# Kernel optimization log

Measured on AMD Instinct MI355X. Metric: run time of the kernel, lower is better.

The kernel has to match this reference:

```python
import jax, jax.numpy as jnp
import numpy as np

B, S, D_IN, D_OUT, N_HEAD = 4, 2048, 1024, 1024, 16
D_HEAD = D_OUT // N_HEAD


def setup_inputs() -> dict:
    key = jax.random.key(0)
    k_x, k_wq, k_wo, k_bo = jax.random.split(key, 4)
    x = jax.random.normal(k_x, (B, S, D_IN), dtype=jnp.float32)
    # nn.Linear(d_in, d_out) weight is [d_out, d_in]; we store transposed [d_in, d_out]
    W_Q = jax.random.normal(k_wq, (D_IN, D_OUT), dtype=jnp.float32) * (D_IN ** -0.5)
    W_out = jax.random.normal(k_wo, (D_OUT, D_OUT), dtype=jnp.float32) * (D_OUT ** -0.5)
    b_out = jax.random.normal(k_bo, (D_OUT,), dtype=jnp.float32) * 0.01
    return {"x": x, "W_Q": W_Q, "W_out": W_out, "b_out": b_out}


def reference(x, W_Q, W_out, b_out):
    b, n_tok, _ = x.shape
    # Faithful to source: Q, K, V all use W_Q (source bug preserved)
    qkv = jnp.einsum('btd,de->bte', x, W_Q)  # [b, s, d_out]
    q = qkv.reshape(b, n_tok, N_HEAD, D_HEAD).transpose(0, 2, 1, 3)  # [b,h,s,dh]
    k = q
    v = q
    scores = jnp.einsum('bhqd,bhkd->bhqk', q, k)  # [b,h,s,s]
    causal = jnp.triu(jnp.ones((n_tok, n_tok), dtype=bool), k=1)
    scores = jnp.where(causal, -jnp.inf, scores)
    # source divides by sqrt(d_head) after masking; -inf / c == -inf so same result
    attn = jax.nn.softmax(scores / jnp.sqrt(jnp.float32(D_HEAD)), axis=-1)
    ctx = jnp.einsum('bhqk,bhkd->bhqd', attn, v)  # [b,h,s,dh]
    ctx = ctx.transpose(0, 2, 1, 3).reshape(b, n_tok, D_OUT)
    return jnp.einsum('btd,de->bte', ctx, W_out) + b_out
```

## Files before the change

kernel.cpp:

```cpp
#include <hip/hip_runtime.h>
#include <hip/hip_bf16.h>
#include <math.h>

#define B_ 4
#define S_ 2048
#define NH_ 16
#define DH_ 64
#define DM_ 1024

typedef __attribute__((ext_vector_type(4))) float f32x4;
typedef __attribute__((ext_vector_type(8))) short s16x8;
typedef __attribute__((ext_vector_type(4))) short s16x4;
typedef __attribute__((ext_vector_type(2))) unsigned u32x2;

extern "C" __device__ float __ocml_native_exp2_f32(float);
static __device__ __forceinline__ float nexp2(float x) {
  return __ocml_native_exp2_f32(x);
}

static __device__ __forceinline__ short f2bf(float f) {
  union { float f; unsigned u; } c; c.f = f;
  unsigned r = c.u + 0x7fffu + ((c.u >> 16) & 1u);
  return (short)(r >> 16);
}

static __device__ __forceinline__ unsigned pkbf(float a, float b) {
  union { __hip_bfloat162 h; unsigned u; } cv;
  cv.h = __float22bfloat162_rn(make_float2(a, b));
  return cv.u;
}

static __device__ __forceinline__ unsigned pkbf_fast(float a, float b) {
  unsigned r;
  asm("v_cvt_pk_bf16_f32 %0, %1, %2" : "=v"(r) : "v"(a), "v"(b));
  return r;
}

static __device__ __forceinline__ s16x4 mk4(unsigned lo, unsigned hi) {
  union { unsigned u[2]; s16x4 v; } x; x.u[0] = lo; x.u[1] = hi; return x.v;
}

#if __has_builtin(__builtin_amdgcn_mfma_f32_16x16x16bf16_1k)
#define HAVE16 1
static __device__ __forceinline__ f32x4 pv_mfma(s16x4 a, s16x4 b, f32x4 c) {
  return __builtin_amdgcn_mfma_f32_16x16x16bf16_1k(a, b, c, 0, 0, 0);
}
#else
#define HAVE16 0
static __device__ __forceinline__ f32x4 pv_mfma(s16x4 a, s16x4 b, f32x4 c) {
  asm volatile("v_mfma_f32_16x16x16_bf16 %0, %1, %2, %0" : "+v"(c) : "v"(a), "v"(b));
  return c;
}
#endif

static __device__ __forceinline__ void gload16(const void* g, void* l) {
  __builtin_amdgcn_global_load_lds(
      (const __attribute__((address_space(1))) void*)g,
      (__attribute__((address_space(3))) void*)l, 16, 0, 0);
}

__global__ void cvt_kernel(const float* __restrict__ in, short* __restrict__ out) {
  int i = (blockIdx.x * 256 + threadIdx.x) * 8;
  f32x4 a = *(const f32x4*)(in + i);
  f32x4 b = *(const f32x4*)(in + i + 4);
  s16x8 o;
  o[0] = f2bf(a[0]); o[1] = f2bf(a[1]); o[2] = f2bf(a[2]); o[3] = f2bf(a[3]);
  o[4] = f2bf(b[0]); o[5] = f2bf(b[1]); o[6] = f2bf(b[2]); o[7] = f2bf(b[3]);
  *(s16x8*)(out + i) = o;
}

__global__ void tcvt_kernel(const float* __restrict__ W, short* __restrict__ WT) {
  __shared__ float t[32][33];
  int tx = threadIdx.x & 31, ty = threadIdx.x >> 5;
  int bn = blockIdx.x * 32, bk = blockIdx.y * 32;
#pragma unroll
  for (int r = 0; r < 32; r += 8)
    t[ty + r][tx] = W[(size_t)(bk + ty + r) * DM_ + bn + tx];
  __syncthreads();
#pragma unroll
  for (int r = 0; r < 32; r += 8)
    WT[(size_t)(bn + ty + r) * DM_ + bk + tx] = f2bf(t[tx][ty + r]);
}

template <int EPI>
__global__ __launch_bounds__(256, 2) void gemm_kernel(
    const short* __restrict__ A, const short* __restrict__ BT,
    void* __restrict__ Cout, short* __restrict__ CoutT,
    const float* __restrict__ bias) {
  __shared__ short Al[128 * 64];
  __shared__ short Bl[128 * 64];
  const int tid = threadIdx.x;
  const int wid = tid >> 6, lane = tid & 63;
  const int l15 = lane & 15, l4 = lane >> 4;
  const int bm = blockIdx.y * 128, bn = blockIdx.x * 128;
  const int wm = (wid >> 1) * 64, wn = (wid & 1) * 64;
  f32x4 acc[4][4] = {};

  for (int kt = 0; kt < DM_; kt += 64) {
    __syncthreads();
#pragma unroll
    for (int j = 0; j < 4; ++j) {
      int s = j * 256 + tid;
      int row = s >> 3;
      int sl = (s & 7) ^ (row & 7);
      gload16(A + (size_t)(bm + row) * DM_ + kt + sl * 8, &Al[j * 2048 + wid * 512]);
    }
#pragma unroll
    for (int j = 0; j < 4; ++j) {
      int s = j * 256 + tid;
      int row = s >> 3;
      int sl = (s & 7) ^ (row & 7);
      gload16(BT + (size_t)(bn + row) * DM_ + kt + sl * 8, &Bl[j * 2048 + wid * 512]);
    }
    __syncthreads();
#pragma unroll
    for (int kk = 0; kk < 2; ++kk) {
      s16x8 af[4], bfr[4];
#pragma unroll
      for (int mi = 0; mi < 4; ++mi) {
        int row = wm + mi * 16 + l15;
        int sl = (kk * 4 + l4) ^ (row & 7);
        af[mi] = *(const s16x8*)&Al[row * 64 + sl * 8];
      }
#pragma unroll
      for (int ni = 0; ni < 4; ++ni) {
        int row = wn + ni * 16 + l15;
        int sl = (kk * 4 + l4) ^ (row & 7);
        bfr[ni] = *(const s16x8*)&Bl[row * 64 + sl * 8];
      }
#pragma unroll
      for (int mi = 0; mi < 4; ++mi)
#pragma unroll
        for (int ni = 0; ni < 4; ++ni)
          acc[mi][ni] = __builtin_amdgcn_mfma_f32_16x16x32_bf16(af[mi], bfr[ni], acc[mi][ni], 0, 0, 0);
    }
  }

  if (EPI == 0) {
    const float sc = 0.42466089786f;
    short* Q = (short*)Cout;
#pragma unroll
    for (int mi = 0; mi < 4; ++mi)
#pragma unroll
      for (int ni = 0; ni < 4; ++ni) {
        int rr0 = bm + wm + mi * 16 + l4 * 4;
        int cc = bn + wn + ni * 16 + l15;
        int b = rr0 >> 11, s0 = rr0 & 2047, h = cc >> 6, d = cc & 63;
        int bh = b * NH_ + h;
        float v0 = acc[mi][ni][0] * sc, v1 = acc[mi][ni][1] * sc;
        float v2 = acc[mi][ni][2] * sc, v3 = acc[mi][ni][3] * sc;
        Q[(((size_t)bh * S_ + s0 + 0) << 6) + d] = f2bf(v0);
        Q[(((size_t)bh * S_ + s0 + 1) << 6) + d] = f2bf(v1);
        Q[(((size_t)bh * S_ + s0 + 2) << 6) + d] = f2bf(v2);
        Q[(((size_t)bh * S_ + s0 + 3) << 6) + d] = f2bf(v3);
        u32x2 pk;
        pk[0] = pkbf(v0, v1);
        pk[1] = pkbf(v2, v3);
        *(u32x2*)&CoutT[(((size_t)bh * DH_ + d) << 11) + s0] = pk;
      }
  } else {
    float* O = (float*)Cout;
#pragma unroll
    for (int mi = 0; mi < 4; ++mi)
#pragma unroll
      for (int ni = 0; ni < 4; ++ni)
#pragma unroll
        for (int r = 0; r < 4; ++r) {
          int rr = bm + wm + mi * 16 + l4 * 4 + r;
          int cc = bn + wn + ni * 16 + l15;
          O[(size_t)rr * DM_ + cc] = acc[mi][ni][r] + bias[cc];
        }
  }
}

__global__ __launch_bounds__(256, 4) void attn_kernel(
    const short* __restrict__ Qb, const short* __restrict__ QbT,
    short* __restrict__ Ctx) {
  __shared__ short Kl[2][64 * 64];
  __shared__ short Vt[2][64 * 64];
  const int tid = threadIdx.x;
  const int wid = tid >> 6, lane = tid & 63;
  const int l15 = lane & 15, l4 = lane >> 4;
  const int bid = blockIdx.x;
  const int bh = bid & 63;
  const int g = bid >> 6;
  const int qt = (int)((0x32104567ba98cdefULL >> (g * 4)) & 15);
  const short* Qh = Qb + (size_t)bh * S_ * DH_;
  const short* QTh = QbT + (size_t)bh * DH_ * S_;
  const int q0 = qt * 128 + wid * 32;

  s16x8 aq[2][2];
#pragma unroll
  for (int qi = 0; qi < 2; ++qi)
#pragma unroll
    for (int kk = 0; kk < 2; ++kk)
      aq[qi][kk] = *(const s16x8*)(Qh + (size_t)(q0 + qi * 16 + l15) * DH_ + kk * 32 + l4 * 8);

  f32x4 acc_o[4][2] = {};
  f32x4 lacc[2] = {};
  s16x4 ones;
  ones[0] = (short)0x3F80; ones[1] = (short)0x3F80;
  ones[2] = (short)0x3F80; ones[3] = (short)0x3F80;

  const int e7 = l15 & 7;
  const int ka0 = l15 * 64 + ((l4) ^ e7) * 8;
  const int ka1 = l15 * 64 + ((4 + l4) ^ e7) * 8;
  int vtoff[4];
#pragma unroll
  for (int ki = 0; ki < 4; ++ki)
    vtoff[ki] = l15 * 64 + (((ki * 2 + (l4 >> 1)) ^ e7) << 3) + (l4 & 1) * 4;

  const int c0 = wid * 64 + lane, c1 = c0 + 256;
  const int r0 = c0 >> 3, s0 = (c0 & 7) ^ (r0 & 7);
  const int r1 = c1 >> 3, s1 = (c1 & 7) ^ (r1 & 7);
  const short* pK0 = Qh + r0 * 64 + s0 * 8;
  const short* pK1 = Qh + r1 * 64 + s1 * 8;
  const short* pV0 = QTh + (size_t)r0 * S_ + s0 * 8;
  const short* pV1 = QTh + (size_t)r1 * S_ + s1 * 8;

  auto stage = [&](int buf) {
    gload16(pK0, &Kl[buf][wid * 512]);
    gload16(pK1, &Kl[buf][wid * 512 + 2048]);
    gload16(pV0, &Vt[buf][wid * 512]);
    gload16(pV1, &Vt[buf][wid * 512 + 2048]);
    pK0 += 4096; pK1 += 4096;
    pV0 += 64;   pV1 += 64;
  };

  stage(0);

  int cur = 0;
  const int nt = qt * 2 + 2;
  for (int t = 0; t < nt; ++t) {
    asm volatile("s_waitcnt vmcnt(0)" ::: "memory");
    __syncthreads();
    if (t + 1 < nt) stage(cur ^ 1);
    const int kv0 = t * 64;

    if (kv0 <= q0) {
      const short* kl = &Kl[cur][0];
      const short* vt = &Vt[cur][0];
      f32x4 sa[4][2] = {};
      __builtin_amdgcn_s_setprio(1);
#pragma unroll
      for (int kk = 0; kk < 2; ++kk) {
        const int kb = (kk == 0) ? ka0 : ka1;
        s16x8 ka[4];
#pragma unroll
        for (int ki = 0; ki < 4; ++ki)
          ka[ki] = *(const s16x8*)&kl[kb + ki * 1024];
#pragma unroll
        for (int ki = 0; ki < 4; ++ki)
#pragma unroll
          for (int qi = 0; qi < 2; ++qi)
            sa[ki][qi] = __builtin_amdgcn_mfma_f32_16x16x32_bf16(ka[ki], aq[qi][kk], sa[ki][qi], 0, 0, 0);
      }
      __builtin_amdgcn_s_setprio(0);
      if (kv0 + 63 > q0) {
#pragma unroll
        for (int ki = 0; ki < 4; ++ki)
#pragma unroll
          for (int qi = 0; qi < 2; ++qi)
#pragma unroll
            for (int r = 0; r < 4; ++r) {
              int kvg = kv0 + ki * 16 + l4 * 4 + r;
              int qg = q0 + qi * 16 + l15;
              if (kvg > qg) sa[ki][qi][r] = -INFINITY;
            }
      }
      unsigned pw[4][2][2];
#pragma unroll
      for (int ki = 0; ki < 4; ++ki)
#pragma unroll
        for (int qi = 0; qi < 2; ++qi) {
          float e0 = nexp2(sa[ki][qi][0]);
          float e1 = nexp2(sa[ki][qi][1]);
          float e2 = nexp2(sa[ki][qi][2]);
          float e3 = nexp2(sa[ki][qi][3]);
          pw[ki][qi][0] = pkbf_fast(e0, e1);
          pw[ki][qi][1] = pkbf_fast(e2, e3);
        }
      __builtin_amdgcn_s_setprio(1);
#pragma unroll
      for (int ki = 0; ki < 4; ++ki) {
        lacc[0] = pv_mfma(ones, mk4(pw[ki][0][0], pw[ki][0][1]), lacc[0]);
        lacc[1] = pv_mfma(ones, mk4(pw[ki][1][0], pw[ki][1][1]), lacc[1]);
      }
#pragma unroll
      for (int df = 0; df < 4; ++df) {
#pragma unroll
        for (int ki = 0; ki < 4; ++ki) {
          s16x4 av = *(const s16x4*)&vt[df * 1024 + vtoff[ki]];
          acc_o[df][0] = pv_mfma(av, mk4(pw[ki][0][0], pw[ki][0][1]), acc_o[df][0]);
          acc_o[df][1] = pv_mfma(av, mk4(pw[ki][1][0], pw[ki][1][1]), acc_o[df][1]);
        }
      }
      __builtin_amdgcn_s_setprio(0);
#if !HAVE16
      asm volatile("s_nop 7" :::);
      asm volatile("s_nop 7" :::);
#endif
    }
    cur ^= 1;
  }

  const int b = bh >> 4, h = bh & 15;
  const float ISQC = 2.35482208f;
  float inv[2] = {ISQC / lacc[0][0], ISQC / lacc[1][0]};
#pragma unroll
  for (int df = 0; df < 4; ++df)
#pragma unroll
    for (int qi = 0; qi < 2; ++qi) {
      int qg = q0 + qi * 16 + l15;
      int col = h * 64 + df * 16 + l4 * 4;
      u32x2 pk;
      pk[0] = pkbf_fast(acc_o[df][qi][0] * inv[qi], acc_o[df][qi][1] * inv[qi]);
      pk[1] = pkbf_fast(acc_o[df][qi][2] * inv[qi], acc_o[df][qi][3] * inv[qi]);
      *(u32x2*)&Ctx[(size_t)(b * S_ + qg) * DM_ + col] = pk;
    }
}

extern "C" void kernel_launch(void* const* d_in, const int* in_sizes, int n_in,
                              void* d_out, int out_size, void* d_ws, size_t ws_size,
                              hipStream_t stream) {
  const float* x  = (const float*)d_in[0];
  const float* Wq = (const float*)d_in[1];
  const float* Wo = (const float*)d_in[2];
  const float* bo = (const float*)d_in[3];
  float* out = (float*)d_out;
  char* ws = (char*)d_ws;

  short* xb  = (short*)(ws);
  short* WqT = (short*)(ws + 16777216);
  short* WoT = (short*)(ws + 18874368);
  short* Qb  = (short*)(ws + 20971520);
  short* QbT = (short*)(ws + 37748736);
  short* Ctx = xb;

  cvt_kernel<<<4096, 256, 0, stream>>>(x, xb);
  tcvt_kernel<<<dim3(32, 32), 256, 0, stream>>>(Wq, WqT);
  tcvt_kernel<<<dim3(32, 32), 256, 0, stream>>>(Wo, WoT);
  gemm_kernel<0><<<dim3(8, 64), 256, 0, stream>>>(xb, WqT, Qb, QbT, nullptr);
  attn_kernel<<<1024, 256, 0, stream>>>(Qb, QbT, Ctx);
  gemm_kernel<1><<<dim3(8, 64), 256, 0, stream>>>(Ctx, WoT, out, nullptr, bo);
}
```

Before: 122.2 us.

## Halve attention query tile to 64 rows and merge weight transpose launches

The attention kernel now gives each block 64 query rows (16 per wave) instead of 128 (32 per wave) and launches 2048 blocks, scheduled longest-first. This gives finer causal load balance and removes the per-wave skip branch. The cost is that each K/V tile loaded into LDS is reused by half as many queries, roughly doubling K/V traffic. The two weight transpose-convert launches are merged into one grid with a z dimension, and the Q epilogue reuses the packed hardware bf16 conversion instead of converting each value twice.

New measurement: 123.3 us. Within noise of the previous version (+0.9%).

```diff
diff --git a/kernel.cpp b/kernel.cpp
--- a/kernel.cpp
+++ b/kernel.cpp
@@ -22,12 +22,6 @@
   union { float f; unsigned u; } c; c.f = f;
   unsigned r = c.u + 0x7fffu + ((c.u >> 16) & 1u);
   return (short)(r >> 16);
-}
-
-static __device__ __forceinline__ unsigned pkbf(float a, float b) {
-  union { __hip_bfloat162 h; unsigned u; } cv;
-  cv.h = __float22bfloat162_rn(make_float2(a, b));
-  return cv.u;
 }
 
 static __device__ __forceinline__ unsigned pkbf_fast(float a, float b) {
@@ -69,8 +63,11 @@
   *(s16x8*)(out + i) = o;
 }
 
-__global__ void tcvt_kernel(const float* __restrict__ W, short* __restrict__ WT) {
+__global__ void tcvt_kernel(const float* __restrict__ W0, const float* __restrict__ W1,
+                            short* __restrict__ T0, short* __restrict__ T1) {
   __shared__ float t[32][33];
+  const float* W = blockIdx.z ? W1 : W0;
+  short* WT = blockIdx.z ? T1 : T0;
   int tx = threadIdx.x & 31, ty = threadIdx.x >> 5;
   int bn = blockIdx.x * 32, bk = blockIdx.y * 32;
 #pragma unroll
@@ -147,15 +144,13 @@
         int cc = bn + wn + ni * 16 + l15;
         int b = rr0 >> 11, s0 = rr0 & 2047, h = cc >> 6, d = cc & 63;
         int bh = b * NH_ + h;
-        float v0 = acc[mi][ni][0] * sc, v1 = acc[mi][ni][1] * sc;
-        float v2 = acc[mi][ni][2] * sc, v3 = acc[mi][ni][3] * sc;
-        Q[(((size_t)bh * S_ + s0 + 0) << 6) + d] = f2bf(v0);
-        Q[(((size_t)bh * S_ + s0 + 1) << 6) + d] = f2bf(v1);
-        Q[(((size_t)bh * S_ + s0 + 2) << 6) + d] = f2bf(v2);
-        Q[(((size_t)bh * S_ + s0 + 3) << 6) + d] = f2bf(v3);
         u32x2 pk;
-        pk[0] = pkbf(v0, v1);
-        pk[1] = pkbf(v2, v3);
+        pk[0] = pkbf_fast(acc[mi][ni][0] * sc, acc[mi][ni][1] * sc);
+        pk[1] = pkbf_fast(acc[mi][ni][2] * sc, acc[mi][ni][3] * sc);
+        Q[(((size_t)bh * S_ + s0 + 0) << 6) + d] = (short)(pk[0] & 0xffff);
+        Q[(((size_t)bh * S_ + s0 + 1) << 6) + d] = (short)(pk[0] >> 16);
+        Q[(((size_t)bh * S_ + s0 + 2) << 6) + d] = (short)(pk[1] & 0xffff);
+        Q[(((size_t)bh * S_ + s0 + 3) << 6) + d] = (short)(pk[1] >> 16);
         *(u32x2*)&CoutT[(((size_t)bh * DH_ + d) << 11) + s0] = pk;
       }
   } else {
@@ -183,21 +178,18 @@
   const int l15 = lane & 15, l4 = lane >> 4;
   const int bid = blockIdx.x;
   const int bh = bid & 63;
-  const int g = bid >> 6;
-  const int qt = (int)((0x32104567ba98cdefULL >> (g * 4)) & 15);
+  const int s = 31 - (bid >> 6);
   const short* Qh = Qb + (size_t)bh * S_ * DH_;
   const short* QTh = QbT + (size_t)bh * DH_ * S_;
-  const int q0 = qt * 128 + wid * 32;
-
-  s16x8 aq[2][2];
-#pragma unroll
-  for (int qi = 0; qi < 2; ++qi)
-#pragma unroll
-    for (int kk = 0; kk < 2; ++kk)
-      aq[qi][kk] = *(const s16x8*)(Qh + (size_t)(q0 + qi * 16 + l15) * DH_ + kk * 32 + l4 * 8);
-
-  f32x4 acc_o[4][2] = {};
-  f32x4 lacc[2] = {};
+  const int q0 = s * 64 + wid * 16;
+
+  s16x8 aq[2];
+#pragma unroll
+  for (int kk = 0; kk < 2; ++kk)
+    aq[kk] = *(const s16x8*)(Qh + (size_t)(q0 + l15) * DH_ + kk * 32 + l4 * 8);
+
+  f32x4 acc_o[4] = {};
+  f32x4 lacc = {};
   s16x4 ones;
   ones[0] = (short)0x3F80; ones[1] = (short)0x3F80;
   ones[2] = (short)0x3F80; ones[3] = (short)0x3F80;
@@ -230,94 +222,82 @@
   stage(0);
 
   int cur = 0;
-  const int nt = qt * 2 + 2;
+  const int nt = s + 1;
   for (int t = 0; t < nt; ++t) {
     asm volatile("s_waitcnt vmcnt(0)" ::: "memory");
     __syncthreads();
     if (t + 1 < nt) stage(cur ^ 1);
     const int kv0 = t * 64;
-
-    if (kv0 <= q0) {
-      const short* kl = &Kl[cur][0];
-      const short* vt = &Vt[cur][0];
-      f32x4 sa[4][2] = {};
-      __builtin_amdgcn_s_setprio(1);
-#pragma unroll
-      for (int kk = 0; kk < 2; ++kk) {
-        const int kb = (kk == 0) ? ka0 : ka1;
-        s16x8 ka[4];
-#pragma unroll
-        for (int ki = 0; ki < 4; ++ki)
-          ka[ki] = *(const s16x8*)&kl[kb + ki * 1024];
-#pragma unroll
-        for (int ki = 0; ki < 4; ++ki)
-#pragma unroll
-          for (int qi = 0; qi < 2; ++qi)
-            sa[ki][qi] = __builtin_amdgcn_mfma_f32_16x16x32_bf16(ka[ki], aq[qi][kk], sa[ki][qi], 0, 0, 0);
+    const short* kl = &Kl[cur][0];
+    const short* vt = &Vt[cur][0];
+
+    f32x4 sa[4] = {};
+    __builtin_amdgcn_s_setprio(1);
+#pragma unroll
+    for (int kk = 0; kk < 2; ++kk) {
+      const int kb = (kk == 0) ? ka0 : ka1;
+      s16x8 ka[4];
+#pragma unroll
+      for (int ki = 0; ki < 4; ++ki)
+        ka[ki] = *(const s16x8*)&kl[kb + ki * 1024];
+#pragma unroll
+      for (int ki = 0; ki < 4; ++ki)
+        sa[ki] = __builtin_amdgcn_mfma_f32_16x16x32_bf16(ka[ki], aq[kk], sa[ki], 0, 0, 0);
+    }
+    __builtin_amdgcn_s_setprio(0);
+
+    if (kv0 + 63 > q0) {
+      int qg = q0 + l15;
+#pragma unroll
+      for (int ki = 0; ki < 4; ++ki)
+#pragma unroll
+        for (int r = 0; r < 4; ++r)
+          if (kv0 + ki * 16 + l4 * 4 + r > qg) sa[ki][r] = -INFINITY;
+    }
+
+    unsigned pw[4][2];
+#pragma unroll
+    for (int ki = 0; ki < 4; ++ki) {
+      float e0 = nexp2(sa[ki][0]);
+      float e1 = nexp2(sa[ki][1]);
+      float e2 = nexp2(sa[ki][2]);
+      float e3 = nexp2(sa[ki][3]);
+      pw[ki][0] = pkbf_fast(e0, e1);
+      pw[ki][1] = pkbf_fast(e2, e3);
+    }
+
+    __builtin_amdgcn_s_setprio(1);
+#pragma unroll
+    for (int ki = 0; ki < 4; ++ki)
+      lacc = pv_mfma(ones, mk4(pw[ki][0], pw[ki][1]), lacc);
+#pragma unroll
+    for (int df = 0; df < 4; ++df) {
+#pragma unroll
+      for (int ki = 0; ki < 4; ++ki) {
+        s16x4 av = *(const s16x4*)&vt[df * 1024 + vtoff[ki]];
+        acc_o[df] = pv_mfma(av, mk4(pw[ki][0], pw[ki][1]), acc_o[df]);
       }
-      __builtin_amdgcn_s_setprio(0);
-      if (kv0 + 63 > q0) {
-#pragma unroll
-        for (int ki = 0; ki < 4; ++ki)
-#pragma unroll
-          for (int qi = 0; qi < 2; ++qi)
-#pragma unroll
-            for (int r = 0; r < 4; ++r) {
-              int kvg = kv0 + ki * 16 + l4 * 4 + r;
-              int qg = q0 + qi * 16 + l15;
-              if (kvg > qg) sa[ki][qi][r] = -INFINITY;
-            }
-      }
-      unsigned pw[4][2][2];
-#pragma unroll
-      for (int ki = 0; ki < 4; ++ki)
-#pragma unroll
-        for (int qi = 0; qi < 2; ++qi) {
-          float e0 = nexp2(sa[ki][qi][0]);
-          float e1 = nexp2(sa[ki][qi][1]);
-          float e2 = nexp2(sa[ki][qi][2]);
-          float e3 = nexp2(sa[ki][qi][3]);
-          pw[ki][qi][0] = pkbf_fast(e0, e1);
-          pw[ki][qi][1] = pkbf_fast(e2, e3);
-        }
-      __builtin_amdgcn_s_setprio(1);
-#pragma unroll
-      for (int ki = 0; ki < 4; ++ki) {
-        lacc[0] = pv_mfma(ones, mk4(pw[ki][0][0], pw[ki][0][1]), lacc[0]);
-        lacc[1] = pv_mfma(ones, mk4(pw[ki][1][0], pw[ki][1][1]), lacc[1]);
-      }
-#pragma unroll
-      for (int df = 0; df < 4; ++df) {
-#pragma unroll
-        for (int ki = 0; ki < 4; ++ki) {
-          s16x4 av = *(const s16x4*)&vt[df * 1024 + vtoff[ki]];
-          acc_o[df][0] = pv_mfma(av, mk4(pw[ki][0][0], pw[ki][0][1]), acc_o[df][0]);
-          acc_o[df][1] = pv_mfma(av, mk4(pw[ki][1][0], pw[ki][1][1]), acc_o[df][1]);
-        }
-      }
-      __builtin_amdgcn_s_setprio(0);
+    }
+    __builtin_amdgcn_s_setprio(0);
 #if !HAVE16
-      asm volatile("s_nop 7" :::);
-      asm volatile("s_nop 7" :::);
+    asm volatile("s_nop 7" :::);
+    asm volatile("s_nop 7" :::);
 #endif
-    }
     cur ^= 1;
   }
 
   const int b = bh >> 4, h = bh & 15;
   const float ISQC = 2.35482208f;
-  float inv[2] = {ISQC / lacc[0][0], ISQC / lacc[1][0]};
-#pragma unroll
-  for (int df = 0; df < 4; ++df)
-#pragma unroll
-    for (int qi = 0; qi < 2; ++qi) {
-      int qg = q0 + qi * 16 + l15;
-      int col = h * 64 + df * 16 + l4 * 4;
-      u32x2 pk;
-      pk[0] = pkbf_fast(acc_o[df][qi][0] * inv[qi], acc_o[df][qi][1] * inv[qi]);
-      pk[1] = pkbf_fast(acc_o[df][qi][2] * inv[qi], acc_o[df][qi][3] * inv[qi]);
-      *(u32x2*)&Ctx[(size_t)(b * S_ + qg) * DM_ + col] = pk;
-    }
+  float inv = ISQC / lacc[0];
+  int qg = q0 + l15;
+#pragma unroll
+  for (int df = 0; df < 4; ++df) {
+    int col = h * 64 + df * 16 + l4 * 4;
+    u32x2 pk;
+    pk[0] = pkbf_fast(acc_o[df][0] * inv, acc_o[df][1] * inv);
+    pk[1] = pkbf_fast(acc_o[df][2] * inv, acc_o[df][3] * inv);
+    *(u32x2*)&Ctx[(size_t)(b * S_ + qg) * DM_ + col] = pk;
+  }
 }
 
 extern "C" void kernel_launch(void* const* d_in, const int* in_sizes, int n_in,
@@ -338,9 +318,8 @@
   short* Ctx = xb;
 
   cvt_kernel<<<4096, 256, 0, stream>>>(x, xb);
-  tcvt_kernel<<<dim3(32, 32), 256, 0, stream>>>(Wq, WqT);
-  tcvt_kernel<<<dim3(32, 32), 256, 0, stream>>>(Wo, WoT);
+  tcvt_kernel<<<dim3(32, 32, 2), 256, 0, stream>>>(Wq, Wo, WqT, WoT);
   gemm_kernel<0><<<dim3(8, 64), 256, 0, stream>>>(xb, WqT, Qb, QbT, nullptr);
-  attn_kernel<<<1024, 256, 0, stream>>>(Qb, QbT, Ctx);
+  attn_kernel<<<2048, 256, 0, stream>>>(Qb, QbT, Ctx);
   gemm_kernel<1><<<dim3(8, 64), 256, 0, stream>>>(Ctx, WoT, out, nullptr, bo);
 }
```
